# Kernel optimization log

Hardware: AMD Instinct MI355X
Metric: run time of the kernel (lower is better)

Reference implementation:

```python
import jax, jax.numpy as jnp
import numpy as np
import math

HIDDEN = 768
HEADS = 12
HEAD_DIM = HIDDEN // HEADS
BLOCK = 256
TOPK = 3
BATCH = 2
SEQ = 2048


def setup_inputs() -> dict:
    key = jax.random.key(0)
    ks = jax.random.split(key, 5)
    s = 1.0 / math.sqrt(HIDDEN)
    return {
        "hidden_states": jax.random.normal(ks[0], (BATCH, SEQ, HIDDEN), jnp.float32),
        "Wq": jax.random.normal(ks[1], (HIDDEN, HIDDEN), jnp.float32) * s,
        "Wk": jax.random.normal(ks[2], (HIDDEN, HIDDEN), jnp.float32) * s,
        "Wv": jax.random.normal(ks[3], (HIDDEN, HIDDEN), jnp.float32) * s,
        "Wo": jax.random.normal(ks[4], (HIDDEN, HIDDEN), jnp.float32) * s,
    }


def _rope(x, sin, cos):
    # x: [B, H, S, D]; rotate-half RoPE
    d2 = x.shape[-1] // 2
    x1, x2 = x[..., :d2], x[..., d2:]
    return x * cos + jnp.concatenate([-x2, x1], axis=-1) * sin


def reference(hidden_states, Wq, Wk, Wv, Wo):
    B, S, Hd = hidden_states.shape
    H, D, bs, K = HEADS, HEAD_DIM, BLOCK, TOPK
    nb = S // bs  # number of key blocks
    scale = 1.0 / math.sqrt(D)

    def split_heads(x):
        return x.reshape(B, S, H, D).transpose(0, 2, 1, 3)  # [B,H,S,D]

    q = split_heads(hidden_states @ Wq.T)
    k = split_heads(hidden_states @ Wk.T)
    v = split_heads(hidden_states @ Wv.T)

    # rotary embedding (standard rotate-half RoPE, base 10000)
    inv_freq = 1.0 / (10000.0 ** (jnp.arange(0, D, 2, dtype=jnp.float32) / D))
    ang = jnp.arange(S, dtype=jnp.float32)[:, None] * inv_freq[None, :]  # [S, D/2]
    emb = jnp.concatenate([ang, ang], axis=-1)  # [S, D]
    sin, cos = jnp.sin(emb), jnp.cos(emb)
    q = _rope(q, sin, cos)
    k = _rope(k, sin, cos)

    # mean-pooled block representations of keys: [B,H,nb,D]
    block_reps = k.reshape(B, H, nb, bs, D).mean(axis=3)

    # routing scores: per-token score against each block rep
    bscores = jnp.einsum('bhsd,bhnd->bhsn', q, block_reps) * scale  # [B,H,S,nb]
    pos = jnp.arange(S)
    cur = pos // bs                       # current block of each query, [S]
    blk = jnp.arange(nb)
    future = blk[None, None, None, :] > cur[None, None, :, None]
    bscores = jnp.where(future, -jnp.inf, bscores)
    # current block is force-selected (score set to dtype max)
    is_cur = blk[None, None, None, :] == cur[None, None, :, None]
    bscores = jnp.where(is_cur, jnp.finfo(bscores.dtype).max, bscores)

    _, topk_idx = jax.lax.top_k(bscores, min(K, nb))  # [B,H,S,K]
    selected = jnp.sum(jax.nn.one_hot(topk_idx, nb, dtype=jnp.float32), axis=-2) > 0  # [B,H,S,nb]

    # per-key-position mask: key t allowed iff its block is selected for query i,
    # and within the current block only t <= i (matches original truncation).
    sel_t = selected[:, :, :, cur]                          # [B,H,Sq,Sk]
    intra_ok = (cur[None, :] != cur[:, None]) | (pos[None, :] <= pos[:, None])  # [Sq,Sk]
    mask = sel_t & intra_ok[None, None]

    scores = jnp.einsum('bhqd,bhkd->bhqk', q, k) * scale
    scores = jnp.where(mask, scores, -jnp.inf)
    probs = jax.nn.softmax(scores, axis=-1)
    out = jnp.einsum('bhqk,bhkd->bhqd', probs, v)

    out = out.transpose(0, 2, 1, 3).reshape(B, S, Hd)
    return out @ Wo.T
```

## Files before the change

### kernel.cpp

```cpp
#include <hip/hip_runtime.h>
#include <math.h>


#define HID   768
#define NH    12
#define DH    64
#define SEQN  2048
#define BATCH 2
#define NTOK  (BATCH*SEQN)
#define NB    8
#define BLKSZ 256
#define NEG_INF (-__builtin_huge_valf())
#define POS_INF (__builtin_huge_valf())
#define LO_SCALE 2048.0f
#define LO_INV   (1.0f/2048.0f)
#define EXP2C    0.18033688f

#define SPLIT_ROWS 1024
#define NBH   (BATCH*NH)

typedef unsigned short u16;
typedef _Float16 v8hf __attribute__((ext_vector_type(8)));
typedef float    v4f  __attribute__((ext_vector_type(4)));

__device__ __forceinline__ u16 f2h(float x) {
    _Float16 h = (_Float16)x;
    return __builtin_bit_cast(u16, h);
}
__device__ __forceinline__ float h2f(u16 u) {
    return (float)__builtin_bit_cast(_Float16, u);
}
__device__ __forceinline__ v8hf ldhf8(const u16* p) {
    return *reinterpret_cast<const v8hf*>(p);
}
__device__ __forceinline__ void g2lds16(const u16* g, u16* l) {
    __builtin_amdgcn_global_load_lds(
        (const __attribute__((address_space(1))) void*)g,
        (__attribute__((address_space(3))) void*)l, 16, 0, 0);
}
#define MFMA16(a, b, c) __builtin_amdgcn_mfma_f32_16x16x32_f16(a, b, c, 0, 0, 0)

__global__ __launch_bounds__(256)
void preproc_k(const float* __restrict__ X,  const float* __restrict__ Wq,
               const float* __restrict__ Wk, const float* __restrict__ Wv,
               const float* __restrict__ Wo, float2* __restrict__ tab,
               u16* __restrict__ Xh, u16* __restrict__ Xl,
               u16* __restrict__ Wq2, u16* __restrict__ Wk2,
               u16* __restrict__ Wv2, u16* __restrict__ Wo2)
{
    const int NW = HID * HID;
    const int id = blockIdx.x;
    const int tid = threadIdx.x;
    if (id < 12288) {
        const int i = id * 256 + tid;
        const float x = X[i];
        const u16 h = f2h(x);
        Xh[i] = h;
        Xl[i] = f2h((x - h2f(h)) * LO_SCALE);
    } else if (id < 21504) {
        const int j = (id - 12288) * 256 + tid;
        const int z = j / NW, i = j - z * NW;
        const float* src = (z == 0) ? Wq : (z == 1) ? Wk : (z == 2) ? Wv : Wo;
        u16* dst = (z == 0) ? Wq2 : (z == 1) ? Wk2 : (z == 2) ? Wv2 : Wo2;
        const float x = src[i];
        const u16 h = f2h(x);
        dst[i] = h;
        dst[i + NW] = f2h((x - h2f(h)) * LO_SCALE);
    } else {
        const int i = (id - 21504) * 256 + tid;
        const int s = i >> 5, f = i & 31;
        const double y  = exp((double)f * (log(10000.0) / 32.0));
        const float yf = (float)y;
        const float invf = 1.0f / yf;
        const float ang  = (float)s * invf;
        tab[i] = make_float2((float)sin((double)ang), (float)cos((double)ang));
    }
}

__device__ __forceinline__
void qkv_mainloop(const u16* __restrict__ Ah, const u16* __restrict__ Al,
                  const u16* __restrict__ Bh, const u16* __restrict__ Bl,
                  int m0, int nb0, int c_start,
                  u16* As, u16* Bs, v4f acc[2][4])
{
    const int tid = threadIdx.x;
    const int w = tid >> 6, lane = tid & 63;
    const int col = lane & 15, quad = lane >> 4;

    int a_row[4], a_gl[4];
    #pragma unroll
    for (int r = 0; r < 4; r++) {
        const int g = r * 256 + tid;
        a_row[r] = g >> 3;
        a_gl[r]  = (g & 7) ^ (a_row[r] & 7);
    }
    int b_row[2], b_gl[2];
    #pragma unroll
    for (int r = 0; r < 2; r++) {
        const int g = r * 256 + tid;
        b_row[r] = g >> 3;
        b_gl[r]  = (g & 7) ^ (b_row[r] & 7);
    }

    for (int c = c_start; c < 3; c++) {
        const u16* Ap = (c == 0) ? Al : Ah;
        const u16* Bp = (c == 1) ? Bl : Bh;
        for (int itc = 0; itc < HID / 64; itc++) {
            const int k0 = itc * 64;
            __syncthreads();
            #pragma unroll
            for (int r = 0; r < 4; r++)
                g2lds16(Ap + (size_t)(m0 + a_row[r]) * HID + k0 + a_gl[r] * 8,
                        &As[(r * 256 + w * 64) * 8]);
            #pragma unroll
            for (int r = 0; r < 2; r++)
                g2lds16(Bp + (size_t)(nb0 + b_row[r]) * HID + k0 + b_gl[r] * 8,
                        &Bs[(r * 256 + w * 64) * 8]);
            __syncthreads();
            #pragma unroll
            for (int ks = 0; ks < 2; ks++) {
                v8hf af[2], bf_[4];
                #pragma unroll
                for (int mt = 0; mt < 2; mt++) {
                    const int row = w * 32 + mt * 16 + col;
                    const int gph = (ks * 4 + quad) ^ (row & 7);
                    af[mt] = ldhf8(&As[row * 64 + gph * 8]);
                }
                #pragma unroll
                for (int nt = 0; nt < 4; nt++) {
                    const int row = nt * 16 + col;
                    const int gph = (ks * 4 + quad) ^ (row & 7);
                    bf_[nt] = ldhf8(&Bs[row * 64 + gph * 8]);
                }
                #pragma unroll
                for (int mt = 0; mt < 2; mt++)
                    #pragma unroll
                    for (int nt = 0; nt < 4; nt++)
                        acc[mt][nt] = MFMA16(af[mt], bf_[nt], acc[mt][nt]);
            }
        }
        if (c == 1) {
            #pragma unroll
            for (int mt = 0; mt < 2; mt++)
                #pragma unroll
                for (int nt = 0; nt < 4; nt++)
                    #pragma unroll
                    for (int r = 0; r < 4; r++)
                        acc[mt][nt][r] *= LO_INV;
        }
    }
    __syncthreads();
}

__global__ __launch_bounds__(256)
void qkv_fused_gemm_k(const u16* __restrict__ Xh, const u16* __restrict__ Xl,
                      const u16* __restrict__ Wq2, const u16* __restrict__ Wk2,
                      const u16* __restrict__ Wv2, const float2* __restrict__ tab,
                      float* __restrict__ q32, u16* __restrict__ kh16,
                      u16* __restrict__ vth, float* __restrict__ partial)
{
    __shared__ u16 As[128 * 64];
    __shared__ u16 Bs[64 * 64];
    __shared__ float psum[4][64];

    const int NW = HID * HID;
    const int id    = blockIdx.x;
    const int xcd   = id & 7, loc = id >> 3;
    const int mtile = xcd * 4 + (loc & 3);
    const int ntile = loc >> 2;
    const int m0  = mtile * 128;
    const int mat = ntile / 12;
    const int nb0 = (ntile - mat * 12) * 64;
    const u16* Bh = (mat == 0) ? Wq2 : (mat == 1) ? Wk2 : Wv2;

    v4f acc[2][4] = {};
    qkv_mainloop(Xh, Xl, Bh, Bh + NW, m0, nb0, (mat == 2) ? 1 : 0, As, Bs, acc);

    const int tid = threadIdx.x;
    const int w = tid >> 6, lane = tid & 63;
    const int col = lane & 15, quad = lane >> 4;
    const int b = m0 >> 11;
    const int h = nb0 >> 6;
    const size_t bh = (size_t)b * NH + h;

    if (mat == 2) {
        #pragma unroll
        for (int nt = 0; nt < 4; nt++) {
            const int d = nt * 16 + col;
            #pragma unroll
            for (int mt = 0; mt < 2; mt++) {
                const int m = m0 + w * 32 + mt * 16 + quad * 4;
                const int s = m & (SEQN - 1);
                ushort4 pk = make_ushort4(f2h(acc[mt][nt][0]), f2h(acc[mt][nt][1]),
                                          f2h(acc[mt][nt][2]), f2h(acc[mt][nt][3]));
                *(ushort4*)&vth[(bh * DH + d) * SEQN + s] = pk;
            }
        }
        return;
    }

    float vsum[4] = {0.f, 0.f, 0.f, 0.f};
    #pragma unroll
    for (int mt = 0; mt < 2; mt++) {
        #pragma unroll
        for (int nt = 0; nt < 4; nt++) {
            const int d = nt * 16 + col;
            #pragma unroll
            for (int r = 0; r < 4; r++) {
                const int m = m0 + w * 32 + mt * 16 + quad * 4 + r;
                const int s = m & (SEQN - 1);
                const float part = acc[mt][nt ^ 2][r];
                const float2 sc = tab[(s << 5) + (d & 31)];
                const float val = (d < 32) ? acc[mt][nt][r] * sc.y - part * sc.x
                                           : acc[mt][nt][r] * sc.y + part * sc.x;
                const size_t idx = (bh * SEQN + s) * DH + d;
                if (mat == 0) {
                    q32[idx] = val;
                } else {
                    kh16[idx] = f2h(val);
                    vsum[nt] += val;
                }
            }
        }
    }
    if (mat == 1) {
        #pragma unroll
        for (int nt = 0; nt < 4; nt++) {
            float v = vsum[nt];
            v += __shfl_xor(v, 16);
            v += __shfl_xor(v, 32);
            if (quad == 0) psum[w][nt * 16 + col] = v;
        }
        __syncthreads();
        if (tid < 64) {
            const float s4 = (psum[0][tid] + psum[1][tid])
                           + (psum[2][tid] + psum[3][tid]);
            const int nblk = (m0 & (SEQN - 1)) >> 8;
            const int half = (m0 >> 7) & 1;
            partial[((bh * NB + nblk) * 2 + half) * 64 + tid] = s4;
        }
    }
}

__global__ __launch_bounds__(256)
void out_gemm_mfma_k(const u16* __restrict__ Ah, const u16* __restrict__ Wo2,
                     float* __restrict__ C)
{
    __shared__ u16 As[64 * 64];
    __shared__ u16 Bs[64 * 64];

    const int NW = HID * HID;
    const int id    = blockIdx.x;
    const int xcd   = id & 7, loc = id >> 3;
    const int mtile = xcd * 8 + (loc & 7);
    const int ntile = loc >> 3;
    const int m0 = mtile * 64, n0 = ntile * 64;
    const int tid = threadIdx.x;
    const int w = tid >> 6, lane = tid & 63;
    const int col = lane & 15, quad = lane >> 4;

    const int r0 = tid >> 3,         gl0 = (tid & 7) ^ (r0 & 7);
    const int r1 = (256 + tid) >> 3, gl1 = ((256 + tid) & 7) ^ (r1 & 7);

    v4f acc[4] = {};
    #pragma unroll
    for (int c = 0; c < 2; c++) {
        const u16* Bp = (c == 0) ? (Wo2 + NW) : Wo2;
        for (int itc = 0; itc < HID / 64; itc++) {
            const int k0 = itc * 64;
            __syncthreads();
            g2lds16(Ah + (size_t)(m0 + r0) * HID + k0 + gl0 * 8, &As[(w * 64) * 8]);
            g2lds16(Ah + (size_t)(m0 + r1) * HID + k0 + gl1 * 8, &As[(256 + w * 64) * 8]);
            g2lds16(Bp + (size_t)(n0 + r0) * HID + k0 + gl0 * 8, &Bs[(w * 64) * 8]);
            g2lds16(Bp + (size_t)(n0 + r1) * HID + k0 + gl1 * 8, &Bs[(256 + w * 64) * 8]);
            __syncthreads();
            #pragma unroll
            for (int ks = 0; ks < 2; ks++) {
                const int arow = w * 16 + col;
                v8hf a = ldhf8(&As[arow * 64 + (((ks * 4 + quad) ^ (arow & 7))) * 8]);
                #pragma unroll
                for (int nt = 0; nt < 4; nt++) {
                    const int row = nt * 16 + col;
                    v8hf bb = ldhf8(&Bs[row * 64 + (((ks * 4 + quad) ^ (row & 7))) * 8]);
                    acc[nt] = MFMA16(a, bb, acc[nt]);
                }
            }
        }
        if (c == 0) {
            #pragma unroll
            for (int nt = 0; nt < 4; nt++)
                #pragma unroll
                for (int r = 0; r < 4; r++)
                    acc[nt][r] *= LO_INV;
        }
    }

    #pragma unroll
    for (int nt = 0; nt < 4; nt++)
        #pragma unroll
        for (int r = 0; r < 4; r++) {
            const int m = m0 + w * 16 + quad * 4 + r;
            C[(size_t)m * HID + n0 + nt * 16 + col] = acc[nt][r];
        }
}

__global__ __launch_bounds__(64)
void reps_reduce_k(const float* __restrict__ partial, float* __restrict__ reps)
{
    const int bhn = blockIdx.x;
    const int d = threadIdx.x;
    const float* p = &partial[(size_t)bhn * 128 + d];
    double s = (double)p[0] + (double)p[64];
    reps[(size_t)bhn * 64 + d] = (float)(s * (1.0 / 256.0));
}

__global__ __launch_bounds__(128)
void select_topk_k(const float* __restrict__ qg, const float* __restrict__ reps,
                   unsigned* __restrict__ selm)
{
    __shared__ float rs[NB][DH];
    const int bh = blockIdx.y;
    const int tid = threadIdx.x;
    for (int idx = tid; idx < NB * DH; idx += 128)
        rs[idx >> 6][idx & 63] = reps[(size_t)bh * NB * DH + idx];
    __syncthreads();

    const int qq = blockIdx.x * 128 + tid;
    const float* qv = &qg[((size_t)bh * SEQN + qq) * DH];
    float qr[DH];
    #pragma unroll
    for (int c = 0; c < 16; c++) {
        float4 t = *(const float4*)&qv[c * 4];
        qr[c*4+0]=t.x; qr[c*4+1]=t.y; qr[c*4+2]=t.z; qr[c*4+3]=t.w;
    }
    const int cur = qq >> 8;
    double sc[NB];
    #pragma unroll
    for (int n = 0; n < NB; n++) {
        double ssum = 0.0;
        for (int d = 0; d < DH; d++) ssum += (double)qr[d] * (double)rs[n][d];
        sc[n] = ssum * 0.125;
    }
    for (int n = cur + 1; n < NB; n++) sc[n] = -1e300;
    sc[cur] = 1e300;
    unsigned mask = 0;
    for (int p = 0; p < 3; p++) {
        int bi = -1; double bv = 0.0;
        for (int n = 0; n < NB; n++) {
            if ((mask >> n) & 1) continue;
            if (bi < 0 || sc[n] > bv) { bi = n; bv = sc[n]; }
        }
        mask |= 1u << bi;
    }
    selm[(size_t)bh * SEQN + qq] = mask;
}

__global__ __launch_bounds__(256, 4)
void moba_attn_k(const float* __restrict__ q32, const u16* __restrict__ kh16,
                 const u16* __restrict__ vth, const unsigned* __restrict__ selm,
                 u16* __restrict__ aoh, float* __restrict__ po,
                 float* __restrict__ ml)
{
    __shared__ u16 kbuf[2][64 * 64];
    __shared__ u16 vbuf[2][64 * 64];
    __shared__ u16 plds[4][16][64];
    unsigned* s_uni = (unsigned*)&vbuf[1][0];

    const int id  = blockIdx.x;
    const int xcd = id & 7, loc = id >> 3;
    const int bh  = xcd * 3 + loc / 48;
    const int u   = loc % 48;
    int qb, split, stride;
    if (u < 16) { qb = u;                 split = 0;          stride = 1; }
    else        { qb = 16 + ((u - 16) >> 1); split = (u - 16) & 1; stride = 2; }
    const int q0  = qb * 64;
    const int cur = q0 >> 8;
    const int tid = threadIdx.x;
    const int wave = tid >> 6, lane = tid & 63;
    const int col = lane & 15, quad = lane >> 4;
    const int qw0 = q0 + wave * 16;
    const int qpos = qw0 + col;
    const size_t bhS = (size_t)bh * SEQN;
    const size_t bhV = (size_t)bh * DH;

    if (tid == 0) *s_uni = 0;
    __syncthreads();
    const unsigned mymask = selm[bhS + qw0 + col];
    unsigned uw = mymask;
    #pragma unroll
    for (int off = 1; off < 16; off <<= 1) uw |= __shfl_xor(uw, off);
    if (lane == 0) atomicOr(s_uni, uw);
    const unsigned wmask = __builtin_amdgcn_readfirstlane(uw);

    v8hf qh[2], ql[2];
    #pragma unroll
    for (int ks = 0; ks < 2; ks++) {
        const float* qp = &q32[(bhS + qw0 + col) * DH + ks * 32 + quad * 8];
        float4 f0 = *(const float4*)qp;
        float4 f1 = *(const float4*)(qp + 4);
        float qf[8] = {f0.x, f0.y, f0.z, f0.w, f1.x, f1.y, f1.z, f1.w};
        union { u16 u[8]; v8hf h; } uh, ul;
        #pragma unroll
        for (int j = 0; j < 8; j++) {
            u16 hb = f2h(qf[j]);
            uh.u[j] = hb;
            ul.u[j] = f2h((qf[j] - h2f(hb)) * LO_SCALE);
        }
        qh[ks] = uh.h; ql[ks] = ul.h;
    }
    __syncthreads();
    const unsigned uni = __builtin_amdgcn_readfirstlane(*s_uni);

    int n_nxt = __builtin_ctz(uni), c_nxt = 0;
    bool has_nxt = true;
    auto c2max = [&](int n) { return (n == cur) ? ((q0 + 63 - n * BLKSZ) >> 6) : 3; };
    auto advance1 = [&]() {
        if (c_nxt < c2max(n_nxt)) { c_nxt++; return; }
        for (int nn = n_nxt + 1; nn < NB; nn++)
            if ((uni >> nn) & 1) { n_nxt = nn; c_nxt = 0; return; }
        has_nxt = false;
    };
    for (int i = 0; i < split; i++) if (has_nxt) advance1();
    int n_cur = n_nxt, c_cur = c_nxt;
    const bool cur_valid = has_nxt;

    const size_t srow0 = (size_t)bh * SPLIT_ROWS + (q0 - SPLIT_ROWS);

    if (!cur_valid) {
        if (stride == 2) {
            if (quad == 0) {
                const size_t r = srow0 + wave * 16 + col;
                ml[(r * 2 + split) * 2 + 0] = NEG_INF;
                ml[(r * 2 + split) * 2 + 1] = 0.f;
            }
            #pragma unroll
            for (int nt = 0; nt < 4; nt++)
                #pragma unroll
                for (int r = 0; r < 4; r++) {
                    const size_t rq = srow0 + wave * 16 + quad * 4 + r;
                    po[(rq * 2 + split) * 64 + nt * 16 + col] = 0.f;
                }
        }
        return;
    }
    for (int i = 0; i < stride; i++) if (has_nxt) advance1();

    const int sg_row0 = tid >> 3;
    const int sg_gl0  = (tid & 7) ^ (sg_row0 & 7);
    const int sg_row1 = (256 + tid) >> 3;
    const int sg_gl1  = ((256 + tid) & 7) ^ (sg_row1 & 7);
    auto stage = [&](int n, int c2, int buf) {
        const int kb = n * BLKSZ + c2 * 64;
        u16* kd = (u16*)kbuf[buf];
        u16* vd = (u16*)vbuf[buf];
        const size_t ks0 = (bhS + kb + sg_row0) * DH + sg_gl0 * 8;
        const size_t ks1 = (bhS + kb + sg_row1) * DH + sg_gl1 * 8;
        const size_t vs0 = (bhV + sg_row0) * SEQN + kb + sg_gl0 * 8;
        const size_t vs1 = (bhV + sg_row1) * SEQN + kb + sg_gl1 * 8;
        g2lds16(kh16 + ks0, kd + (wave * 64) * 8);
        g2lds16(kh16 + ks1, kd + (256 + wave * 64) * 8);
        g2lds16(vth + vs0, vd + (wave * 64) * 8);
        g2lds16(vth + vs1, vd + (256 + wave * 64) * 8);
    };

    const v4f zero4 = {0.f, 0.f, 0.f, 0.f};
    v4f oacc[4] = {zero4, zero4, zero4, zero4};
    float m_i = NEG_INF, l_i = 0.f;
    const int psw = (col & 7) << 1;

    stage(n_cur, c_cur, 0);
    int t = 0;
    while (true) {
        __syncthreads();
        if (has_nxt) stage(n_nxt, c_nxt, (t + 1) & 1);

        const int n  = n_cur;
        if ((wmask >> n) & 1) {
            const int kb = n * BLKSZ + c_cur * 64;
            const bool iscur = (n == cur);
            const float selinf = ((mymask >> n) & 1) ? 0.f : POS_INF;
            const bool need_mask = iscur && (kb + 63 > qw0);
            const u16* kd = (const u16*)kbuf[t & 1];
            const u16* vd = (const u16*)vbuf[t & 1];

            v4f sf[4];
            __builtin_amdgcn_s_setprio(1);
            #pragma unroll
            for (int mt = 0; mt < 4; mt++) {
                const int row = mt * 16 + col;
                const int r7 = row & 7;
                v8hf kh0 = ldhf8(&kd[(row * 8 + (quad ^ r7)) * 8]);
                v8hf kh1 = ldhf8(&kd[(row * 8 + ((4 + quad) ^ r7)) * 8]);
                v4f c = zero4;
                c = MFMA16(kh0, ql[0], c);
                c = MFMA16(kh1, ql[1], c);
                #pragma unroll
                for (int r = 0; r < 4; r++) c[r] *= LO_INV;
                c = MFMA16(kh0, qh[0], c);
                c = MFMA16(kh1, qh[1], c);
                sf[mt] = c;
            }
            __builtin_amdgcn_s_setprio(0);

            if (need_mask) {
                #pragma unroll
                for (int mt = 0; mt < 4; mt++)
                    #pragma unroll
                    for (int r = 0; r < 4; r++) {
                        const int kidx = kb + mt * 16 + quad * 4 + r;
                        sf[mt][r] = (kidx <= qpos) ? sf[mt][r] : NEG_INF;
                    }
            }

            float rm = NEG_INF;
            #pragma unroll
            for (int mt = 0; mt < 4; mt++)
                #pragma unroll
                for (int r = 0; r < 4; r++) rm = fmaxf(rm, sf[mt][r]);
            rm = fmaxf(rm, __shfl_xor(rm, 16));
            rm = fmaxf(rm, __shfl_xor(rm, 32));
            rm = rm - selinf;
            const float mnew  = fmaxf(m_i, rm);
            const float alpha = (m_i == NEG_INF) ? 0.f : exp2f((m_i - mnew) * EXP2C);
            const float biasC = ((mnew == NEG_INF) ? 0.f : mnew * EXP2C) + selinf;

            float lsum = 0.f;
            #pragma unroll
            for (int mt = 0; mt < 4; mt++) {
                ushort4 hv;
                #pragma unroll
                for (int r = 0; r < 4; r++) {
                    float p = exp2f(fmaf(sf[mt][r], EXP2C, -biasC));
                    lsum += p;
                    u16 hu = f2h(p);
                    if (r == 0) hv.x = hu;
                    else if (r == 1) hv.y = hu;
                    else if (r == 2) hv.z = hu;
                    else hv.w = hu;
                }
                *(ushort4*)&plds[wave][col][((mt * 4 + quad) ^ psw) * 4] = hv;
            }
            lsum += __shfl_xor(lsum, 16);
            lsum += __shfl_xor(lsum, 32);
            l_i = l_i * alpha + lsum;
            m_i = mnew;

            float ar[4];
            #pragma unroll
            for (int r = 0; r < 4; r++) ar[r] = __shfl(alpha, quad * 4 + r, 16);
            #pragma unroll
            for (int nt = 0; nt < 4; nt++)
                #pragma unroll
                for (int r = 0; r < 4; r++) oacc[nt][r] *= ar[r];

            __threadfence_block();

            __builtin_amdgcn_s_setprio(1);
            #pragma unroll
            for (int ks2 = 0; ks2 < 2; ks2++) {
                v8hf ph = ldhf8(&plds[wave][col][((ks2 * 8 + quad * 2) ^ psw) * 4]);
                #pragma unroll
                for (int nt = 0; nt < 4; nt++) {
                    const int row = nt * 16 + col;
                    const int g = (ks2 * 4 + quad) ^ (row & 7);
                    v8hf vh = ldhf8(&vd[(row * 8 + g) * 8]);
                    oacc[nt] = MFMA16(ph, vh, oacc[nt]);
                }
            }
            __builtin_amdgcn_s_setprio(0);
        }

        if (!has_nxt) break;
        n_cur = n_nxt; c_cur = c_nxt;
        for (int i = 0; i < stride; i++) if (has_nxt) advance1();
        t++;
    }

    if (stride == 2) {
        if (quad == 0) {
            const size_t r = srow0 + wave * 16 + col;
            ml[(r * 2 + split) * 2 + 0] = m_i;
            ml[(r * 2 + split) * 2 + 1] = l_i;
        }
        #pragma unroll
        for (int nt = 0; nt < 4; nt++)
            #pragma unroll
            for (int r = 0; r < 4; r++) {
                const size_t rq = srow0 + wave * 16 + quad * 4 + r;
                po[(rq * 2 + split) * 64 + nt * 16 + col] = oacc[nt][r];
            }
        return;
    }

    const int b = bh / NH, h = bh % NH;
    const float invl = 1.f / l_i;
    float ir[4];
    #pragma unroll
    for (int r = 0; r < 4; r++) ir[r] = __shfl(invl, quad * 4 + r, 16);
    #pragma unroll
    for (int nt = 0; nt < 4; nt++)
        #pragma unroll
        for (int r = 0; r < 4; r++) {
            const int qi = qw0 + quad * 4 + r;
            const size_t idx = ((size_t)b * SEQN + qi) * HID + h * DH + nt * 16 + col;
            aoh[idx] = f2h(oacc[nt][r] * ir[r]);
        }
}

__global__ __launch_bounds__(256)
void attn_combine_k(const float* __restrict__ po, const float* __restrict__ ml,
                    u16* __restrict__ aoh)
{
    const int g = blockIdx.x * 256 + threadIdx.x;
    const int d = g & 63;
    const size_t row = (size_t)(g >> 6);
    const int bh = (int)(row >> 10);
    const int qlocal = (int)(row & 1023);
    const float m0 = ml[(row * 2 + 0) * 2 + 0], l0 = ml[(row * 2 + 0) * 2 + 1];
    const float m1 = ml[(row * 2 + 1) * 2 + 0], l1 = ml[(row * 2 + 1) * 2 + 1];
    const float m  = fmaxf(m0, m1);
    const float a0 = (m0 == NEG_INF) ? 0.f : exp2f((m0 - m) * EXP2C);
    const float a1 = (m1 == NEG_INF) ? 0.f : exp2f((m1 - m) * EXP2C);
    const float o  = po[(row * 2 + 0) * 64 + d] * a0
                   + po[(row * 2 + 1) * 64 + d] * a1;
    const float inv = 1.f / (l0 * a0 + l1 * a1);
    const int b = bh / NH, h = bh % NH;
    const int q = SPLIT_ROWS + qlocal;
    aoh[((size_t)b * SEQN + q) * HID + h * DH + d] = f2h(o * inv);
}

extern "C" void kernel_launch(void* const* d_in, const int* in_sizes, int n_in,
                              void* d_out, int out_size, void* d_ws, size_t ws_size,
                              hipStream_t stream)
{
    const float* X  = (const float*)d_in[0];
    const float* Wq = (const float*)d_in[1];
    const float* Wk = (const float*)d_in[2];
    const float* Wv = (const float*)d_in[3];
    const float* Wo = (const float*)d_in[4];
    float* out = (float*)d_out;

    char* p = (char*)d_ws;
    float* q32 = (float*)p;                p += (size_t)NTOK*HID*4;
    u16* kh16 = (u16*)p;                   p += (size_t)NTOK*HID*2;
    u16* vth  = (u16*)p;                   p += (size_t)NTOK*HID*2;
    u16* Xh   = (u16*)p;                   p += (size_t)NTOK*HID*2;
    u16* Xl   = (u16*)p;                   p += (size_t)NTOK*HID*2;
    u16* Wq2  = (u16*)p;                   p += (size_t)HID*HID*2*2;
    u16* Wk2  = (u16*)p;                   p += (size_t)HID*HID*2*2;
    u16* Wv2  = (u16*)p;                   p += (size_t)HID*HID*2*2;
    u16* Wo2  = (u16*)p;                   p += (size_t)HID*HID*2*2;
    float* partial = (float*)p;            p += (size_t)BATCH*NH*NB*2*64*4;
    float* reps    = (float*)p;            p += (size_t)BATCH*NH*NB*DH*4;
    unsigned* selm = (unsigned*)p;         p += (size_t)BATCH*NH*SEQN*4;
    float2* tab    = (float2*)p;           p += (size_t)SEQN*32*8;
    u16* aoh = Xh;

    float* po = (float*)Xl;
    float* ml = po + (size_t)NBH * SPLIT_ROWS * 2 * 64;

    preproc_k<<<dim3(21760), 256, 0, stream>>>(X, Wq, Wk, Wv, Wo, tab,
                                               Xh, Xl, Wq2, Wk2, Wv2, Wo2);

    qkv_fused_gemm_k<<<dim3(1152), 256, 0, stream>>>(
        Xh, Xl, Wq2, Wk2, Wv2, tab, q32, kh16, vth, partial);

    reps_reduce_k<<<dim3(BATCH*NH*NB), 64, 0, stream>>>(partial, reps);
    select_topk_k<<<dim3(SEQN/128, BATCH*NH), 128, 0, stream>>>(q32, reps, selm);

    moba_attn_k<<<dim3(1152), 256, 0, stream>>>(
        q32, kh16, vth, selm, aoh, po, ml);

    attn_combine_k<<<dim3(6144), 256, 0, stream>>>(po, ml, aoh);

    out_gemm_mfma_k<<<dim3(768), 256, 0, stream>>>(aoh, Wo2, out);
}
```

Before: 227.0 us.

## Single-buffer V tile loaded during QK compute and raise occupancy target

```diff
diff --git a/kernel.cpp b/kernel.cpp
--- a/kernel.cpp
+++ b/kernel.cpp
@@ -355,16 +355,16 @@
     selm[(size_t)bh * SEQN + qq] = mask;
 }
 
-__global__ __launch_bounds__(256, 4)
+__global__ __launch_bounds__(256, 5)
 void moba_attn_k(const float* __restrict__ q32, const u16* __restrict__ kh16,
                  const u16* __restrict__ vth, const unsigned* __restrict__ selm,
                  u16* __restrict__ aoh, float* __restrict__ po,
                  float* __restrict__ ml)
 {
     __shared__ u16 kbuf[2][64 * 64];
-    __shared__ u16 vbuf[2][64 * 64];
+    __shared__ u16 vbuf[64 * 64];
     __shared__ u16 plds[4][16][64];
-    unsigned* s_uni = (unsigned*)&vbuf[1][0];
+    unsigned* s_uni = (unsigned*)&plds[0][0][0];
 
     const int id  = blockIdx.x;
     const int xcd = id & 7, loc = id >> 3;
@@ -449,18 +449,17 @@
     const int sg_gl0  = (tid & 7) ^ (sg_row0 & 7);
     const int sg_row1 = (256 + tid) >> 3;
     const int sg_gl1  = ((256 + tid) & 7) ^ (sg_row1 & 7);
-    auto stage = [&](int n, int c2, int buf) {
+    auto stage_k = [&](int n, int c2, int buf) {
         const int kb = n * BLKSZ + c2 * 64;
         u16* kd = (u16*)kbuf[buf];
-        u16* vd = (u16*)vbuf[buf];
-        const size_t ks0 = (bhS + kb + sg_row0) * DH + sg_gl0 * 8;
-        const size_t ks1 = (bhS + kb + sg_row1) * DH + sg_gl1 * 8;
-        const size_t vs0 = (bhV + sg_row0) * SEQN + kb + sg_gl0 * 8;
-        const size_t vs1 = (bhV + sg_row1) * SEQN + kb + sg_gl1 * 8;
-        g2lds16(kh16 + ks0, kd + (wave * 64) * 8);
-        g2lds16(kh16 + ks1, kd + (256 + wave * 64) * 8);
-        g2lds16(vth + vs0, vd + (wave * 64) * 8);
-        g2lds16(vth + vs1, vd + (256 + wave * 64) * 8);
+        g2lds16(kh16 + (bhS + kb + sg_row0) * DH + sg_gl0 * 8, kd + (wave * 64) * 8);
+        g2lds16(kh16 + (bhS + kb + sg_row1) * DH + sg_gl1 * 8, kd + (256 + wave * 64) * 8);
+    };
+    auto stage_v = [&](int n, int c2) {
+        const int kb = n * BLKSZ + c2 * 64;
+        u16* vd = (u16*)vbuf;
+        g2lds16(vth + (bhV + sg_row0) * SEQN + kb + sg_gl0 * 8, vd + (wave * 64) * 8);
+        g2lds16(vth + (bhV + sg_row1) * SEQN + kb + sg_gl1 * 8, vd + (256 + wave * 64) * 8);
     };
 
     const v4f zero4 = {0.f, 0.f, 0.f, 0.f};
@@ -468,20 +467,28 @@
     float m_i = NEG_INF, l_i = 0.f;
     const int psw = (col & 7) << 1;
 
-    stage(n_cur, c_cur, 0);
+    stage_k(n_cur, c_cur, 0);
     int t = 0;
     while (true) {
-        __syncthreads();
-        if (has_nxt) stage(n_nxt, c_nxt, (t + 1) & 1);
+        asm volatile("s_waitcnt lgkmcnt(0)" ::: "memory");
+        __builtin_amdgcn_s_barrier();
+        __builtin_amdgcn_sched_barrier(0);
+
+        stage_v(n_cur, c_cur);
+        if (has_nxt) stage_k(n_nxt, c_nxt, (t + 1) & 1);
+        else         stage_k(n_cur, c_cur, (t + 1) & 1);
+
+        asm volatile("s_waitcnt vmcnt(4)" ::: "memory");
+        __builtin_amdgcn_sched_barrier(0);
 
         const int n  = n_cur;
-        if ((wmask >> n) & 1) {
+        const bool act = (wmask >> n) & 1;
+        if (act) {
             const int kb = n * BLKSZ + c_cur * 64;
             const bool iscur = (n == cur);
             const float selinf = ((mymask >> n) & 1) ? 0.f : POS_INF;
             const bool need_mask = iscur && (kb + 63 > qw0);
             const u16* kd = (const u16*)kbuf[t & 1];
-            const u16* vd = (const u16*)vbuf[t & 1];
 
             v4f sf[4];
             __builtin_amdgcn_s_setprio(1);
@@ -554,7 +561,13 @@
                 for (int r = 0; r < 4; r++) oacc[nt][r] *= ar[r];
 
             __threadfence_block();
-
+        }
+
+        asm volatile("s_waitcnt vmcnt(2)" ::: "memory");
+        __builtin_amdgcn_sched_barrier(0);
+
+        if (act) {
+            const u16* vd = (const u16*)vbuf;
             __builtin_amdgcn_s_setprio(1);
             #pragma unroll
             for (int ks2 = 0; ks2 < 2; ks2++) {
```

New measurement: 241.8 us. 6.5% more time.
